# Optimization experiments

Hardware: AMD Instinct MI355X
Metric: run time of the kernel (lower is better)

The kernel has to match this reference:

```python
import jax, jax.numpy as jnp
import numpy as np

N_NODES = 50000
N_EDGES = 800000
IN_CH = 3
HID = 32
OUT_CH = 16
HEADS = 8
NEG_SLOPE = 0.2  # PyG GATConv default LeakyReLU slope


def setup_inputs() -> dict:
    key = jax.random.key(0)
    ks = jax.random.split(key, 12)
    x = jax.random.normal(ks[0], (N_NODES, IN_CH), dtype=jnp.float32)
    edge_index = jax.random.randint(ks[1], (2, N_EDGES), 0, N_NODES, dtype=jnp.int64)
    # Layer 1: GATConv(3 -> 32, heads=8, concat=True)
    s1 = 1.0 / np.sqrt(IN_CH)
    W1 = jax.random.uniform(ks[2], (IN_CH, HEADS * HID), jnp.float32, -s1, s1)
    att_src1 = jax.random.uniform(ks[3], (HEADS, HID), jnp.float32, -s1, s1)
    att_dst1 = jax.random.uniform(ks[4], (HEADS, HID), jnp.float32, -s1, s1)
    bias1 = jnp.zeros((HEADS * HID,), jnp.float32)
    # Layer 2: GATConv(256 -> 16, heads=1, concat=False)
    s2 = 1.0 / np.sqrt(HEADS * HID)
    W2 = jax.random.uniform(ks[5], (HEADS * HID, 1 * OUT_CH), jnp.float32, -s2, s2)
    att_src2 = jax.random.uniform(ks[6], (1, OUT_CH), jnp.float32, -s2, s2)
    att_dst2 = jax.random.uniform(ks[7], (1, OUT_CH), jnp.float32, -s2, s2)
    bias2 = jnp.zeros((OUT_CH,), jnp.float32)
    return {"x": x, "edge_index": edge_index,
            "W1": W1, "att_src1": att_src1, "att_dst1": att_dst1, "bias1": bias1,
            "W2": W2, "att_src2": att_src2, "att_dst2": att_dst2, "bias2": bias2}


def gat_conv(x, src, dst, W, att_src, att_dst, bias, heads, out_ch, concat):
    """PyG-style GATConv (eval mode: attention dropout is identity).
    src/dst already include self-loops. Returns [N, heads*out_ch] or [N, out_ch]."""
    N = x.shape[0]
    h = (x @ W).reshape(N, heads, out_ch)                      # [N,H,C]
    a_s = jnp.einsum("nhc,hc->nh", h, att_src)                 # [N,H]
    a_d = jnp.einsum("nhc,hc->nh", h, att_dst)                 # [N,H]
    e = jax.nn.leaky_relu(a_s[src] + a_d[dst], NEG_SLOPE)      # [E,H]
    # segment softmax over incoming edges of each dst node
    m = jax.ops.segment_max(e, dst, num_segments=N)            # [N,H]
    e = jnp.exp(e - m[dst])
    denom = jax.ops.segment_sum(e, dst, num_segments=N)        # [N,H]
    alpha = e / (denom[dst] + 1e-16)                           # [E,H]
    msg = h[src] * alpha[:, :, None]                           # [E,H,C]
    out = jax.ops.segment_sum(msg, dst, num_segments=N)        # [N,H,C]
    out = out.reshape(N, heads * out_ch) if concat else out.mean(axis=1)
    return out + bias


def reference(x, edge_index, W1, att_src1, att_dst1, bias1, W2, att_src2, att_dst2, bias2):
    N = x.shape[0]
    loop = jnp.arange(N, dtype=edge_index.dtype)
    src = jnp.concatenate([edge_index[0], loop])  # add self-loops (PyG default)
    dst = jnp.concatenate([edge_index[1], loop])
    h = gat_conv(x, src, dst, W1, att_src1, att_dst1, bias1, HEADS, HID, True)
    h = jax.nn.elu(h)
    out = gat_conv(h, src, dst, W2, att_src2, att_dst2, bias2, 1, OUT_CH, False)
    return out
```

## Files before the change

kernel.cpp:

```cpp
#include <hip/hip_runtime.h>
#include <math.h>

#define N_NODES 50000
#define N_EDGES 800000
#define E_TOT   850000
#define HEADS   8
#define HID     32
#define C1      256
#define OUTC    16
#define NEG     0.2f
#define NB1     ((N_NODES + 255) / 256)

__device__ __forceinline__ float lrelu(float v) { return v > 0.0f ? v : NEG * v; }

__global__ __launch_bounds__(256) void k_setup(
    const float* __restrict__ x, const int* __restrict__ ei,
    const float* __restrict__ W1,
    const float* __restrict__ att_s1, const float* __restrict__ att_d1,
    const float* __restrict__ W2,
    const float* __restrict__ att_s2, const float* __restrict__ att_d2,
    float4* __restrict__ xp, int* __restrict__ cnt, int* __restrict__ rank,
    float* __restrict__ As1, float* __restrict__ Ad1,
    float* __restrict__ As2, float* __restrict__ Ad2)
{
    int t = threadIdx.x;
    int e = blockIdx.x * 256 + t;
    if (blockIdx.x == 0) {
        if (t < 24) {
            int k = t / 8, h = t % 8;
            float as = 0.0f, ad = 0.0f;
            for (int c = 0; c < HID; c++) {
                float w = W1[k * C1 + h * HID + c];
                as = fmaf(w, att_s1[h * HID + c], as);
                ad = fmaf(w, att_d1[h * HID + c], ad);
            }
            As1[k * 8 + h] = as; Ad1[k * 8 + h] = ad;
        }
        float as2 = 0.0f, ad2 = 0.0f;
        for (int j = 0; j < OUTC; j++) {
            float w = W2[t * OUTC + j];
            as2 = fmaf(w, att_s2[j], as2);
            ad2 = fmaf(w, att_d2[j], ad2);
        }
        As2[t] = as2; Ad2[t] = ad2;
    }
    if (e < N_NODES)
        xp[e] = make_float4(x[e * 3], x[e * 3 + 1], x[e * 3 + 2], 1.0f);
    if (e < E_TOT) {
        int d = (e < N_EDGES) ? ei[N_EDGES + e] : (e - N_EDGES);
        rank[e] = atomicAdd(&cnt[d], 1);
    }
}

__global__ void k_scan1(const int* __restrict__ cnt, int* __restrict__ part,
                        int* __restrict__ bsum)
{
    __shared__ int s[256];
    int tid = threadIdx.x;
    int i = blockIdx.x * 256 + tid;
    int v = (i < N_NODES) ? cnt[i] : 0;
    s[tid] = v;
    __syncthreads();
    for (int o = 1; o < 256; o <<= 1) {
        int t = (tid >= o) ? s[tid - o] : 0;
        __syncthreads();
        s[tid] += t;
        __syncthreads();
    }
    if (i < N_NODES) part[i] = s[tid] - v;
    if (tid == 255) bsum[blockIdx.x] = s[255];
}

__global__ void k_scan2(int* __restrict__ bsum)
{
    __shared__ int s[256];
    int tid = threadIdx.x;
    int v = (tid < NB1) ? bsum[tid] : 0;
    s[tid] = v;
    __syncthreads();
    for (int o = 1; o < 256; o <<= 1) {
        int t = (tid >= o) ? s[tid - o] : 0;
        __syncthreads();
        s[tid] += t;
        __syncthreads();
    }
    if (tid < NB1) bsum[tid] = s[tid] - v;
}

__global__ void k_scan3(const int* __restrict__ part, const int* __restrict__ bsum,
                        int* __restrict__ off)
{
    int i = blockIdx.x * 256 + threadIdx.x;
    if (i < N_NODES) off[i] = part[i] + bsum[blockIdx.x];
    if (i == 0) off[N_NODES] = E_TOT;
}

__global__ void k_fill(const int* __restrict__ ei, const int* __restrict__ rank,
                       const int* __restrict__ off, int* __restrict__ csr_src)
{
    int e = blockIdx.x * blockDim.x + threadIdx.x;
    if (e >= E_TOT) return;
    int s, d;
    if (e < N_EDGES) { s = ei[e]; d = ei[N_EDGES + e]; } else { s = d = e - N_EDGES; }
    csr_src[off[d] + rank[e]] = s;
}

__global__ __launch_bounds__(256) void k_agg1(
    const int* __restrict__ off, const int* __restrict__ csr_src,
    const float4* __restrict__ xp,
    const float* __restrict__ As1, const float* __restrict__ Ad1,
    float4* __restrict__ xaccw)
{
    int tid = threadIdx.x;
    int h = tid & 7;
    int dst = blockIdx.x * 32 + (tid >> 3);
    if (dst >= N_NODES) return;
    float s0 = As1[h], s1 = As1[8 + h], s2 = As1[16 + h];
    float d0 = Ad1[h], d1 = Ad1[8 + h], d2 = Ad1[16 + h];
    float4 xd = xp[dst];
    float ad = xd.x * d0 + xd.y * d1 + xd.z * d2;
    int beg = off[dst], end = off[dst + 1];
    float a0 = 0.0f, a1 = 0.0f, a2 = 0.0f, a3 = 0.0f;
    int nfull = beg + ((end - beg) & ~7);
    for (int base = beg; base < nfull; base += 8) {
        int sm = csr_src[base + h];
        float4 xv = xp[sm];
        #pragma unroll
        for (int j = 0; j < 8; j++) {
            float vx = __shfl(xv.x, j, 8);
            float vy = __shfl(xv.y, j, 8);
            float vz = __shfl(xv.z, j, 8);
            float as = vx * s0 + vy * s1 + vz * s2;
            float p = __expf(lrelu(as + ad));
            a0 = fmaf(p, vx, a0);
            a1 = fmaf(p, vy, a1);
            a2 = fmaf(p, vz, a2);
            a3 += p;
        }
    }
    if (nfull < end) {
        int idx = nfull + h;
        int sm = (idx < end) ? csr_src[idx] : 0;
        float4 xv = xp[sm];
        int m = end - nfull;
        for (int j = 0; j < m; j++) {
            float vx = __shfl(xv.x, j, 8);
            float vy = __shfl(xv.y, j, 8);
            float vz = __shfl(xv.z, j, 8);
            float as = vx * s0 + vy * s1 + vz * s2;
            float p = __expf(lrelu(as + ad));
            a0 = fmaf(p, vx, a0);
            a1 = fmaf(p, vy, a1);
            a2 = fmaf(p, vz, a2);
            a3 += p;
        }
    }
    xaccw[dst * 8 + h] = make_float4(a0, a1, a2, a3);
}

__global__ __launch_bounds__(256) void k_fin1h2(
    const float4* __restrict__ xaccw, const float* __restrict__ W1,
    const float* __restrict__ b1, const float* __restrict__ W2,
    const float* __restrict__ As2, const float* __restrict__ Ad2,
    float* __restrict__ h2, float* __restrict__ a_s2, float* __restrict__ a_d2)
{
    __shared__ float sW1[3 * C1];
    __shared__ float sAux[3 * C1];
    __shared__ float sW2t[OUTC][260];
    __shared__ float sElu[16][260];
    int t = threadIdx.x;
    for (int i = t; i < 3 * C1; i += 256) sW1[i] = W1[i];
    sAux[t] = b1[t]; sAux[C1 + t] = As2[t]; sAux[2 * C1 + t] = Ad2[t];
    for (int i = t; i < C1 * OUTC; i += 256) {
        int k = i >> 4, j = i & 15;
        sW2t[j][k] = W2[i];
    }
    __syncthreads();
    int n = t >> 4, l = t & 15;
    int node = blockIdx.x * 16 + n;
    float as = 0.0f, ad = 0.0f;
    for (int i = 0; i < 16; i++) {
        int c = l + 16 * i;
        int h = c >> 5;
        float4 xa = xaccw[node * 8 + h];
        float z = (xa.x * sW1[c] + xa.y * sW1[C1 + c] + xa.z * sW1[2 * C1 + c])
                  / (xa.w + 1e-16f) + sAux[c];
        float e = z > 0.0f ? z : expm1f(z);
        sElu[n][c] = e;
        as = fmaf(e, sAux[C1 + c], as);
        ad = fmaf(e, sAux[2 * C1 + c], ad);
    }
    for (int o = 1; o < 16; o <<= 1) {
        as += __shfl_xor(as, o, 64);
        ad += __shfl_xor(ad, o, 64);
    }
    if (l == 0) { a_s2[node] = as; a_d2[node] = ad; }
    __syncthreads();
    const float4* e4 = (const float4*)&sElu[n][0];
    const float4* w4 = (const float4*)&sW2t[l][0];
    float acc = 0.0f;
    #pragma unroll 8
    for (int k = 0; k < 64; k++) {
        float4 a = e4[k], b = w4[k];
        acc = fmaf(a.x, b.x, fmaf(a.y, b.y, fmaf(a.z, b.z, fmaf(a.w, b.w, acc))));
    }
    h2[node * OUTC + l] = acc;
}

__global__ __launch_bounds__(256) void k_agg2(
    const int* __restrict__ off, const int* __restrict__ csr_src,
    const float* __restrict__ a_s, const float* __restrict__ a_d,
    const float* __restrict__ h2, const float* __restrict__ bias,
    float* __restrict__ out)
{
    int tid = threadIdx.x;
    int c = tid & 15;
    int dst = blockIdx.x * 16 + (tid >> 4);
    if (dst >= N_NODES) return;
    int beg = off[dst], end = off[dst + 1];
    float ad = a_d[dst];
    float acc = 0.0f, denp = 0.0f;
    int nfull = beg + ((end - beg) & ~15);
    for (int base = beg; base < nfull; base += 16) {
        int sm = csr_src[base + c];
        float p = __expf(lrelu(a_s[sm] + ad));
        denp += p;
        #pragma unroll
        for (int j = 0; j < 16; j++) {
            int s = __shfl(sm, j, 16);
            float pj = __shfl(p, j, 16);
            acc = fmaf(pj, h2[s * OUTC + c], acc);
        }
    }
    if (nfull < end) {
        int idx = nfull + c;
        int sm = 0; float p = 0.0f;
        if (idx < end) { sm = csr_src[idx]; p = __expf(lrelu(a_s[sm] + ad)); }
        denp += p;
        int m = end - nfull;
        for (int j = 0; j < m; j++) {
            int s = __shfl(sm, j, 16);
            float pj = __shfl(p, j, 16);
            acc = fmaf(pj, h2[s * OUTC + c], acc);
        }
    }
    for (int o = 1; o < 16; o <<= 1) denp += __shfl_xor(denp, o, 16);
    out[dst * OUTC + c] = acc / (denp + 1e-16f) + bias[c];
}

extern "C" void kernel_launch(void* const* d_in, const int* in_sizes, int n_in,
                              void* d_out, int out_size, void* d_ws, size_t ws_size,
                              hipStream_t stream)
{
    (void)in_sizes; (void)n_in; (void)out_size; (void)ws_size;
    const float* x    = (const float*)d_in[0];
    const int*   ei   = (const int*)d_in[1];
    const float* W1   = (const float*)d_in[2];
    const float* as1w = (const float*)d_in[3];
    const float* ad1w = (const float*)d_in[4];
    const float* b1   = (const float*)d_in[5];
    const float* W2   = (const float*)d_in[6];
    const float* as2w = (const float*)d_in[7];
    const float* ad2w = (const float*)d_in[8];
    const float* b2   = (const float*)d_in[9];
    float* out = (float*)d_out;

    const long N = N_NODES;
    char* p = (char*)d_ws;
    auto alloc = [&](size_t elems) {
        void* r = p; p += ((elems + 3) & ~(size_t)3) * 4; return r;
    };

    float4* xp      = (float4*)alloc(N * 4);
    float4* xaccw   = (float4*)alloc(N * HEADS * 4);
    int*   cnt      = (int*)alloc(N);
    int*   part     = (int*)alloc(N);
    int*   off      = (int*)alloc(N + 1);
    int*   bsum     = (int*)alloc(256);
    int*   rank     = (int*)alloc(E_TOT);
    int*   csr_src  = (int*)alloc(E_TOT);
    float* As1      = (float*)alloc(32);
    float* Ad1      = (float*)alloc(32);
    float* As2      = (float*)alloc(C1);
    float* Ad2      = (float*)alloc(C1);
    float* h2v      = (float*)alloc(N * OUTC);
    float* a_s2     = (float*)alloc(N);
    float* a_d2     = (float*)alloc(N);

    hipMemsetAsync(cnt, 0, (size_t)N * sizeof(int), stream);

    k_setup<<<(E_TOT + 255) / 256, 256, 0, stream>>>(
        x, ei, W1, as1w, ad1w, W2, as2w, ad2w,
        xp, cnt, rank, As1, Ad1, As2, Ad2);
    k_scan1<<<NB1, 256, 0, stream>>>(cnt, part, bsum);
    k_scan2<<<1, 256, 0, stream>>>(bsum);
    k_scan3<<<NB1, 256, 0, stream>>>(part, bsum, off);
    k_fill<<<(E_TOT + 255) / 256, 256, 0, stream>>>(ei, rank, off, csr_src);

    k_agg1<<<(int)((N + 31) / 32), 256, 0, stream>>>(off, csr_src, xp, As1, Ad1, xaccw);
    k_fin1h2<<<(int)(N / 16), 256, 0, stream>>>(xaccw, W1, b1, W2, As2, Ad2, h2v, a_s2, a_d2);
    k_agg2<<<(int)((N + 15) / 16), 256, 0, stream>>>(off, csr_src, a_s2, a_d2, h2v, b2, out);
}
```

Baseline: 199.4 us.

## Fuse scan into single-pass lookback, recompute ranks in fill, fuse agg1 with fin

Replaces the three-kernel scan with one decoupled-lookback scan that also resets the counters, so k_fill can recompute each edge's slot with a second atomicAdd instead of storing and reading a rank array. The first-layer aggregation is fused with the layer-1 finalize and layer-2 projection, keeping per-node accumulators in shared memory instead of writing them to global memory and reading them back. This cuts kernel launches and global traffic. The cost is a lookback spin that depends on blocks being scheduled in a workable order, and a fused kernel with more shared memory that may run at lower occupancy.

Result: slower. 236.5 us (+18.6%).

```diff
diff --git a/kernel.cpp b/kernel.cpp
--- a/kernel.cpp
+++ b/kernel.cpp
@@ -19,7 +19,7 @@
     const float* __restrict__ att_s1, const float* __restrict__ att_d1,
     const float* __restrict__ W2,
     const float* __restrict__ att_s2, const float* __restrict__ att_d2,
-    float4* __restrict__ xp, int* __restrict__ cnt, int* __restrict__ rank,
+    float4* __restrict__ xp, int* __restrict__ cnt,
     float* __restrict__ As1, float* __restrict__ Ad1,
     float* __restrict__ As2, float* __restrict__ Ad2)
 {
@@ -48,18 +48,21 @@
         xp[e] = make_float4(x[e * 3], x[e * 3 + 1], x[e * 3 + 2], 1.0f);
     if (e < E_TOT) {
         int d = (e < N_EDGES) ? ei[N_EDGES + e] : (e - N_EDGES);
-        rank[e] = atomicAdd(&cnt[d], 1);
-    }
-}
-
-__global__ void k_scan1(const int* __restrict__ cnt, int* __restrict__ part,
-                        int* __restrict__ bsum)
+        atomicAdd(&cnt[d], 1);
+    }
+}
+
+__global__ __launch_bounds__(256) void k_scan(
+    int* __restrict__ cnt, int* __restrict__ off, unsigned int* __restrict__ state)
 {
     __shared__ int s[256];
+    __shared__ int sbase;
     int tid = threadIdx.x;
-    int i = blockIdx.x * 256 + tid;
-    int v = (i < N_NODES) ? cnt[i] : 0;
-    s[tid] = v;
+    int v = blockIdx.x;
+    int i = v * 256 + tid;
+    int val = (i < N_NODES) ? cnt[i] : 0;
+    if (i < N_NODES) cnt[i] = 0;
+    s[tid] = val;
     __syncthreads();
     for (int o = 1; o < 256; o <<= 1) {
         int t = (tid >= o) ? s[tid - o] : 0;
@@ -67,100 +70,69 @@
         s[tid] += t;
         __syncthreads();
     }
-    if (i < N_NODES) part[i] = s[tid] - v;
-    if (tid == 255) bsum[blockIdx.x] = s[255];
-}
-
-__global__ void k_scan2(int* __restrict__ bsum)
-{
-    __shared__ int s[256];
-    int tid = threadIdx.x;
-    int v = (tid < NB1) ? bsum[tid] : 0;
-    s[tid] = v;
+    int incl = s[tid];
+    int total = s[255];
+    if (tid == 0) {
+        unsigned pub = (v == 0) ? (0x80000000u | (unsigned)total)
+                                : (0x40000000u | (unsigned)total);
+        __hip_atomic_store(&state[v], pub, __ATOMIC_RELEASE, __HIP_MEMORY_SCOPE_AGENT);
+        sbase = 0;
+    }
+    if (v > 0 && tid < 64) {
+        int run = 0, look = v - 1;
+        for (;;) {
+            int idx = look - tid;
+            unsigned st;
+            if (idx >= 0) {
+                do {
+                    st = __hip_atomic_load(&state[idx], __ATOMIC_RELAXED,
+                                           __HIP_MEMORY_SCOPE_AGENT);
+                } while (st == 0u);
+            } else st = 0x80000000u;
+            unsigned long long pm = __ballot((st & 0x80000000u) != 0u);
+            int contrib; bool done;
+            if (pm) {
+                int plane = (int)__ffsll((unsigned long long)pm) - 1;
+                contrib = (tid <= plane) ? (int)(st & 0xFFFFFFu) : 0;
+                done = true;
+            } else {
+                contrib = (int)(st & 0xFFFFFFu);
+                done = false;
+            }
+            for (int o = 32; o > 0; o >>= 1) contrib += __shfl_down(contrib, o);
+            run += __shfl(contrib, 0);
+            if (done) break;
+            look -= 64;
+        }
+        if (tid == 0) {
+            __hip_atomic_store(&state[v], 0x80000000u | (unsigned)(run + total),
+                               __ATOMIC_RELEASE, __HIP_MEMORY_SCOPE_AGENT);
+            sbase = run;
+        }
+    }
     __syncthreads();
-    for (int o = 1; o < 256; o <<= 1) {
-        int t = (tid >= o) ? s[tid - o] : 0;
-        __syncthreads();
-        s[tid] += t;
-        __syncthreads();
-    }
-    if (tid < NB1) bsum[tid] = s[tid] - v;
-}
-
-__global__ void k_scan3(const int* __restrict__ part, const int* __restrict__ bsum,
-                        int* __restrict__ off)
-{
-    int i = blockIdx.x * 256 + threadIdx.x;
-    if (i < N_NODES) off[i] = part[i] + bsum[blockIdx.x];
+    if (i < N_NODES) off[i] = sbase + incl - val;
     if (i == 0) off[N_NODES] = E_TOT;
 }
 
-__global__ void k_fill(const int* __restrict__ ei, const int* __restrict__ rank,
-                       const int* __restrict__ off, int* __restrict__ csr_src)
-{
-    int e = blockIdx.x * blockDim.x + threadIdx.x;
+__global__ __launch_bounds__(256) void k_fill(
+    const int* __restrict__ ei, int* __restrict__ cnt,
+    const int* __restrict__ off, int* __restrict__ csr_src)
+{
+    int e = blockIdx.x * 256 + threadIdx.x;
     if (e >= E_TOT) return;
     int s, d;
     if (e < N_EDGES) { s = ei[e]; d = ei[N_EDGES + e]; } else { s = d = e - N_EDGES; }
-    csr_src[off[d] + rank[e]] = s;
-}
-
-__global__ __launch_bounds__(256) void k_agg1(
+    int r = atomicAdd(&cnt[d], 1);
+    csr_src[off[d] + r] = s;
+}
+
+__global__ __launch_bounds__(256) void k_agg1fin(
     const int* __restrict__ off, const int* __restrict__ csr_src,
     const float4* __restrict__ xp,
     const float* __restrict__ As1, const float* __restrict__ Ad1,
-    float4* __restrict__ xaccw)
-{
-    int tid = threadIdx.x;
-    int h = tid & 7;
-    int dst = blockIdx.x * 32 + (tid >> 3);
-    if (dst >= N_NODES) return;
-    float s0 = As1[h], s1 = As1[8 + h], s2 = As1[16 + h];
-    float d0 = Ad1[h], d1 = Ad1[8 + h], d2 = Ad1[16 + h];
-    float4 xd = xp[dst];
-    float ad = xd.x * d0 + xd.y * d1 + xd.z * d2;
-    int beg = off[dst], end = off[dst + 1];
-    float a0 = 0.0f, a1 = 0.0f, a2 = 0.0f, a3 = 0.0f;
-    int nfull = beg + ((end - beg) & ~7);
-    for (int base = beg; base < nfull; base += 8) {
-        int sm = csr_src[base + h];
-        float4 xv = xp[sm];
-        #pragma unroll
-        for (int j = 0; j < 8; j++) {
-            float vx = __shfl(xv.x, j, 8);
-            float vy = __shfl(xv.y, j, 8);
-            float vz = __shfl(xv.z, j, 8);
-            float as = vx * s0 + vy * s1 + vz * s2;
-            float p = __expf(lrelu(as + ad));
-            a0 = fmaf(p, vx, a0);
-            a1 = fmaf(p, vy, a1);
-            a2 = fmaf(p, vz, a2);
-            a3 += p;
-        }
-    }
-    if (nfull < end) {
-        int idx = nfull + h;
-        int sm = (idx < end) ? csr_src[idx] : 0;
-        float4 xv = xp[sm];
-        int m = end - nfull;
-        for (int j = 0; j < m; j++) {
-            float vx = __shfl(xv.x, j, 8);
-            float vy = __shfl(xv.y, j, 8);
-            float vz = __shfl(xv.z, j, 8);
-            float as = vx * s0 + vy * s1 + vz * s2;
-            float p = __expf(lrelu(as + ad));
-            a0 = fmaf(p, vx, a0);
-            a1 = fmaf(p, vy, a1);
-            a2 = fmaf(p, vz, a2);
-            a3 += p;
-        }
-    }
-    xaccw[dst * 8 + h] = make_float4(a0, a1, a2, a3);
-}
-
-__global__ __launch_bounds__(256) void k_fin1h2(
-    const float4* __restrict__ xaccw, const float* __restrict__ W1,
-    const float* __restrict__ b1, const float* __restrict__ W2,
+    const float* __restrict__ W1, const float* __restrict__ b1,
+    const float* __restrict__ W2,
     const float* __restrict__ As2, const float* __restrict__ Ad2,
     float* __restrict__ h2, float* __restrict__ a_s2, float* __restrict__ a_d2)
 {
@@ -168,43 +140,92 @@
     __shared__ float sAux[3 * C1];
     __shared__ float sW2t[OUTC][260];
     __shared__ float sElu[16][260];
+    __shared__ float4 sXacc[32][8];
     int t = threadIdx.x;
     for (int i = t; i < 3 * C1; i += 256) sW1[i] = W1[i];
     sAux[t] = b1[t]; sAux[C1 + t] = As2[t]; sAux[2 * C1 + t] = Ad2[t];
-    for (int i = t; i < C1 * OUTC; i += 256) {
-        int k = i >> 4, j = i & 15;
-        sW2t[j][k] = W2[i];
-    }
+    for (int i = t; i < C1 * OUTC; i += 256) sW2t[i & 15][i >> 4] = W2[i];
+
+    int h = t & 7;
+    int n8 = t >> 3;
+    int dst = blockIdx.x * 32 + n8;
+    float a0 = 0.0f, a1 = 0.0f, a2 = 0.0f, a3 = 0.0f;
+    if (dst < N_NODES) {
+        float s0 = As1[h], s1 = As1[8 + h], s2 = As1[16 + h];
+        float d0 = Ad1[h], d1 = Ad1[8 + h], d2 = Ad1[16 + h];
+        float4 xd = xp[dst];
+        float ad = xd.x * d0 + xd.y * d1 + xd.z * d2;
+        int beg = off[dst], end = off[dst + 1];
+        int nfull = beg + ((end - beg) & ~7);
+        for (int base = beg; base < nfull; base += 8) {
+            int sm = csr_src[base + h];
+            float4 xv = xp[sm];
+            #pragma unroll
+            for (int j = 0; j < 8; j++) {
+                float vx = __shfl(xv.x, j, 8);
+                float vy = __shfl(xv.y, j, 8);
+                float vz = __shfl(xv.z, j, 8);
+                float as = vx * s0 + vy * s1 + vz * s2;
+                float p = __expf(lrelu(as + ad));
+                a0 = fmaf(p, vx, a0);
+                a1 = fmaf(p, vy, a1);
+                a2 = fmaf(p, vz, a2);
+                a3 += p;
+            }
+        }
+        if (nfull < end) {
+            int idx = nfull + h;
+            int sm = (idx < end) ? csr_src[idx] : 0;
+            float4 xv = xp[sm];
+            int m = end - nfull;
+            for (int j = 0; j < m; j++) {
+                float vx = __shfl(xv.x, j, 8);
+                float vy = __shfl(xv.y, j, 8);
+                float vz = __shfl(xv.z, j, 8);
+                float as = vx * s0 + vy * s1 + vz * s2;
+                float p = __expf(lrelu(as + ad));
+                a0 = fmaf(p, vx, a0);
+                a1 = fmaf(p, vy, a1);
+                a2 = fmaf(p, vz, a2);
+                a3 += p;
+            }
+        }
+    }
+    sXacc[n8][h] = make_float4(a0, a1, a2, a3);
     __syncthreads();
+
     int n = t >> 4, l = t & 15;
-    int node = blockIdx.x * 16 + n;
-    float as = 0.0f, ad = 0.0f;
-    for (int i = 0; i < 16; i++) {
-        int c = l + 16 * i;
-        int h = c >> 5;
-        float4 xa = xaccw[node * 8 + h];
-        float z = (xa.x * sW1[c] + xa.y * sW1[C1 + c] + xa.z * sW1[2 * C1 + c])
-                  / (xa.w + 1e-16f) + sAux[c];
-        float e = z > 0.0f ? z : expm1f(z);
-        sElu[n][c] = e;
-        as = fmaf(e, sAux[C1 + c], as);
-        ad = fmaf(e, sAux[2 * C1 + c], ad);
-    }
-    for (int o = 1; o < 16; o <<= 1) {
-        as += __shfl_xor(as, o, 64);
-        ad += __shfl_xor(ad, o, 64);
-    }
-    if (l == 0) { a_s2[node] = as; a_d2[node] = ad; }
-    __syncthreads();
-    const float4* e4 = (const float4*)&sElu[n][0];
-    const float4* w4 = (const float4*)&sW2t[l][0];
-    float acc = 0.0f;
-    #pragma unroll 8
-    for (int k = 0; k < 64; k++) {
-        float4 a = e4[k], b = w4[k];
-        acc = fmaf(a.x, b.x, fmaf(a.y, b.y, fmaf(a.z, b.z, fmaf(a.w, b.w, acc))));
-    }
-    h2[node * OUTC + l] = acc;
+    #pragma unroll
+    for (int half = 0; half < 2; half++) {
+        int node = blockIdx.x * 32 + half * 16 + n;
+        float as = 0.0f, ad = 0.0f;
+        for (int i = 0; i < 16; i++) {
+            int c = l + 16 * i;
+            float4 xa = sXacc[half * 16 + n][c >> 5];
+            float z = (xa.x * sW1[c] + xa.y * sW1[C1 + c] + xa.z * sW1[2 * C1 + c])
+                      / (xa.w + 1e-16f) + sAux[c];
+            float e = z > 0.0f ? z : expm1f(z);
+            sElu[n][c] = e;
+            as = fmaf(e, sAux[C1 + c], as);
+            ad = fmaf(e, sAux[2 * C1 + c], ad);
+        }
+        for (int o = 1; o < 16; o <<= 1) {
+            as += __shfl_xor(as, o, 64);
+            ad += __shfl_xor(ad, o, 64);
+        }
+        if (l == 0 && node < N_NODES) { a_s2[node] = as; a_d2[node] = ad; }
+        __syncthreads();
+        const float4* e4 = (const float4*)&sElu[n][0];
+        const float4* w4 = (const float4*)&sW2t[l][0];
+        float acc = 0.0f;
+        #pragma unroll 8
+        for (int k = 0; k < 64; k++) {
+            float4 a = e4[k], b = w4[k];
+            acc = fmaf(a.x, b.x, fmaf(a.y, b.y, fmaf(a.z, b.z, fmaf(a.w, b.w, acc))));
+        }
+        if (node < N_NODES) h2[node * OUTC + l] = acc;
+        if (half == 0) __syncthreads();
+    }
 }
 
 __global__ __launch_bounds__(256) void k_agg2(
@@ -271,33 +292,27 @@
         void* r = p; p += ((elems + 3) & ~(size_t)3) * 4; return r;
     };
 
-    float4* xp      = (float4*)alloc(N * 4);
-    float4* xaccw   = (float4*)alloc(N * HEADS * 4);
-    int*   cnt      = (int*)alloc(N);
-    int*   part     = (int*)alloc(N);
-    int*   off      = (int*)alloc(N + 1);
-    int*   bsum     = (int*)alloc(256);
-    int*   rank     = (int*)alloc(E_TOT);
-    int*   csr_src  = (int*)alloc(E_TOT);
-    float* As1      = (float*)alloc(32);
-    float* Ad1      = (float*)alloc(32);
-    float* As2      = (float*)alloc(C1);
-    float* Ad2      = (float*)alloc(C1);
-    float* h2v      = (float*)alloc(N * OUTC);
-    float* a_s2     = (float*)alloc(N);
-    float* a_d2     = (float*)alloc(N);
-
-    hipMemsetAsync(cnt, 0, (size_t)N * sizeof(int), stream);
+    float4*   xp      = (float4*)alloc(N * 4);
+    int*      cnt     = (int*)alloc(N);
+    unsigned* state   = (unsigned*)alloc(256);
+    int*      off     = (int*)alloc(N + 1);
+    int*      csr_src = (int*)alloc(E_TOT);
+    float*    As1     = (float*)alloc(32);
+    float*    Ad1     = (float*)alloc(32);
+    float*    As2     = (float*)alloc(C1);
+    float*    Ad2     = (float*)alloc(C1);
+    float*    h2v     = (float*)alloc(N * OUTC);
+    float*    a_s2    = (float*)alloc(N);
+    float*    a_d2    = (float*)alloc(N);
+
+    hipMemsetAsync(cnt, 0, (size_t)(N + 256) * sizeof(int), stream);
 
     k_setup<<<(E_TOT + 255) / 256, 256, 0, stream>>>(
         x, ei, W1, as1w, ad1w, W2, as2w, ad2w,
-        xp, cnt, rank, As1, Ad1, As2, Ad2);
-    k_scan1<<<NB1, 256, 0, stream>>>(cnt, part, bsum);
-    k_scan2<<<1, 256, 0, stream>>>(bsum);
-    k_scan3<<<NB1, 256, 0, stream>>>(part, bsum, off);
-    k_fill<<<(E_TOT + 255) / 256, 256, 0, stream>>>(ei, rank, off, csr_src);
-
-    k_agg1<<<(int)((N + 31) / 32), 256, 0, stream>>>(off, csr_src, xp, As1, Ad1, xaccw);
-    k_fin1h2<<<(int)(N / 16), 256, 0, stream>>>(xaccw, W1, b1, W2, As2, Ad2, h2v, a_s2, a_d2);
+        xp, cnt, As1, Ad1, As2, Ad2);
+    k_scan<<<NB1, 256, 0, stream>>>(cnt, off, state);
+    k_fill<<<(E_TOT + 255) / 256, 256, 0, stream>>>(ei, cnt, off, csr_src);
+    k_agg1fin<<<(int)((N + 31) / 32), 256, 0, stream>>>(
+        off, csr_src, xp, As1, Ad1, W1, b1, W2, As2, Ad2, h2v, a_s2, a_d2);
     k_agg2<<<(int)((N + 15) / 16), 256, 0, stream>>>(off, csr_src, a_s2, a_d2, h2v, b2, out);
 }
```
